# Performance work log

Hardware: AMD Instinct MI355X
Metric: run time of the kernel (lower is better)

## Reference

```python
import jax, jax.numpy as jnp
import numpy as np

N = 8192       # tokens = batch x seq
D = 2048       # d_model
H = 2048       # per-expert hidden size
E = 8          # num_experts
TOP_K = 2


def setup_inputs() -> dict:
    key = jax.random.key(0)
    ks = jax.random.split(key, 6)
    x = jax.random.normal(ks[0], (N, D), dtype=jnp.float32)
    expert_weights = jax.random.uniform(ks[1], (N, TOP_K), dtype=jnp.float32)
    expert_indices = jax.random.randint(ks[2], (N, TOP_K), 0, E, dtype=jnp.int32)
    batch_size_per_expert = jnp.bincount(expert_indices.reshape(-1), length=E).astype(jnp.int32)
    scale = 0.02
    w1 = jax.random.normal(ks[3], (E, D, H), dtype=jnp.float32) * scale
    w2 = jax.random.normal(ks[4], (E, H, D), dtype=jnp.float32) * scale
    w3 = jax.random.normal(ks[5], (E, D, H), dtype=jnp.float32) * scale
    return {"x": x, "expert_weights": expert_weights, "expert_indices": expert_indices,
            "batch_size_per_expert": batch_size_per_expert, "w1": w1, "w2": w2, "w3": w3}


def reference(x, expert_weights, expert_indices, batch_size_per_expert, w1, w2, w3):
    """Math-equivalent to ParallelMLP.forward_once (non-EP path):
    sort tokens by expert, run per-expert SwiGLU MLP, unpermute and combine
    with top-k routing weights. Output does not depend on the sort order,
    so we express it as: out[t] = sum_k w[t,k] * expert_{idx[t,k]}(x[t]).
    """
    n, d = x.shape
    e = w1.shape[0]
    # Dense combine weights (n, E): scatter top-k routing weights.
    cw = jnp.zeros((n, e), x.dtype).at[jnp.arange(n)[:, None], expert_indices].add(expert_weights)
    out = jnp.zeros_like(x)
    for i in range(e):  # small fixed expert count
        h = jax.nn.silu(x @ w1[i]) * (x @ w3[i])  # (n, H) SwiGLU
        out = out + cw[:, i:i + 1] * (h @ w2[i])
    return out
```

## Files before the change

### kernel.cpp

```cpp
#include <hip/hip_runtime.h>
#include <stdint.h>

typedef unsigned short u16;
typedef __attribute__((ext_vector_type(8))) short s16x8;
typedef __attribute__((ext_vector_type(8))) unsigned short u16x8;
typedef __attribute__((ext_vector_type(4))) float f32x4;

#define N_TOK 8192
#define DDIM 2048
#define HDIM 2048
#define NROWS 16384
#define PADROWS 16640
#define MAXTILES 72
#define KTILES 32

#define W1T_OFF    0ull
#define W3T_OFF    67108864ull
#define W2T_OFF    134217728ull
#define XBF_OFF    201326592ull
#define HS_OFF     234881024ull
#define ROWTOK_OFF 303038464ull
#define POS_OFF    303107072ull
#define META_OFF   303172608ull
#define RES_OFF    0ull
#define WS_NEED    303172736ull

__device__ __forceinline__ u16 f2bf(float f) {
  union { float f; unsigned u; } v; v.f = f;
  unsigned r = v.u + 0x7fffu + ((v.u >> 16) & 1u);
  return (u16)(r >> 16);
}
__device__ __forceinline__ float bf2f(u16 u) {
  union { unsigned u; float f; } v; v.u = ((unsigned)u) << 16; return v.f;
}
__device__ __forceinline__ void gload_lds16(const u16* g, u16* l) {
  __builtin_amdgcn_global_load_lds(
      (const __attribute__((address_space(1))) unsigned int*)g,
      (__attribute__((address_space(3))) unsigned int*)l, 16, 0, 0);
}

__global__ void r1_kernel(const int* __restrict__ bsz, int* __restrict__ meta,
                          int* __restrict__ rowtok) {
  if (threadIdx.x == 0) {
    int off = 0, tbv = 0;
    meta[8] = 0; meta[17] = 0;
    for (int e = 0; e < 8; ++e) {
      meta[e] = 0;
      int c = bsz[e];
      off += c;  meta[9 + e] = off;
      tbv += (c + 255) >> 8; meta[18 + e] = tbv;
    }
  }
  for (int p = NROWS + (int)threadIdx.x; p < PADROWS; p += 256) rowtok[p] = 0;
}

__global__ void r2_kernel(const int* __restrict__ eidx, int* __restrict__ meta,
                          int* __restrict__ rowtok, int* __restrict__ posOf) {
  int i = blockIdx.x * 256 + threadIdx.x;
  int e = eidx[i];
  int p = atomicAdd(&meta[e], 1);
  int row = meta[8 + e] + p;
  rowtok[row] = i >> 1;
  posOf[i] = row;
}

__global__ void convert_x_kernel(const float* __restrict__ x, u16* __restrict__ xbf) {
  long long c = blockIdx.x * 256 + threadIdx.x;
  const float4 v0 = *(const float4*)&x[c * 8];
  const float4 v1 = *(const float4*)&x[c * 8 + 4];
  u16x8 u;
  u[0] = f2bf(v0.x); u[1] = f2bf(v0.y); u[2] = f2bf(v0.z); u[3] = f2bf(v0.w);
  u[4] = f2bf(v1.x); u[5] = f2bf(v1.y); u[6] = f2bf(v1.z); u[7] = f2bf(v1.w);
  *(u16x8*)&xbf[c * 8] = u;
}

__global__ __launch_bounds__(256) void transpose_cvt_kernel(
    const float* __restrict__ w1, const float* __restrict__ w2, const float* __restrict__ w3,
    u16* __restrict__ w1T, u16* __restrict__ w2T, u16* __restrict__ w3T) {
  __shared__ float tile[64][65];
  int z = blockIdx.z;
  const float* src; u16* dst;
  if (z < 8)        { src = w1 + (size_t)z * 4194304;        dst = w1T + (size_t)z * 4194304; }
  else if (z < 16)  { src = w3 + (size_t)(z - 8) * 4194304;  dst = w3T + (size_t)(z - 8) * 4194304; }
  else              { src = w2 + (size_t)(z - 16) * 4194304; dst = w2T + (size_t)(z - 16) * 4194304; }
  int r0 = blockIdx.y * 64, c0 = blockIdx.x * 64;
  int tid = threadIdx.x;
  int lr = tid >> 4, lc4 = (tid & 15) * 4;
#pragma unroll
  for (int i = 0; i < 4; ++i) {
    const float4 v = *(const float4*)&src[(size_t)(r0 + lr + i * 16) * 2048 + c0 + lc4];
    tile[lr + i * 16][lc4 + 0] = v.x; tile[lr + i * 16][lc4 + 1] = v.y;
    tile[lr + i * 16][lc4 + 2] = v.z; tile[lr + i * 16][lc4 + 3] = v.w;
  }
  __syncthreads();
  int orb = tid >> 3, oc8 = (tid & 7) * 8;
#pragma unroll
  for (int i = 0; i < 2; ++i) {
    int orow = orb + i * 32;
    u16x8 u;
#pragma unroll
    for (int j = 0; j < 8; ++j) u[j] = f2bf(tile[oc8 + j][orow]);
    *(u16x8*)&dst[(size_t)(c0 + orow) * 2048 + r0 + oc8] = u;
  }
}

template<int EPI>
__device__ __forceinline__ void gemm_body(
    const u16* __restrict__ A, const u16* __restrict__ B1m, const u16* __restrict__ B3m,
    const int* __restrict__ gather, const int* __restrict__ meta, u16* __restrict__ out) {
  const int* offs = meta + 8;
  const int* tb = meta + 17;

  const int NCOLB = EPI ? 16 : 8;
  const int CG = NCOLB / 4;
  const int nper = (MAXTILES * NCOLB) / 8;
  const int lin = (int)blockIdx.x;
  const int w = (lin & 7) * nper + (lin >> 3);
  const int sb = w >> 5, t5 = w & 31;
  const int tileId = (sb / CG) * 8 + (t5 >> 2);
  const int colb = (sb % CG) * 4 + (t5 & 3);

  if (tileId >= tb[8]) return;
  int e = 0;
#pragma unroll
  for (int qq = 1; qq < 8; ++qq) if (tileId >= tb[qq]) e = qq;
  const int row0 = offs[e] + (tileId - tb[e]) * 256;
  const int vr = offs[e + 1] - row0;

  const int bRowA = EPI ? colb * 128 : colb * 256;
  const int bRowB = EPI ? colb * 128 : colb * 256 + 128;

  __shared__ u16 lds[2][4][8192];

  const int tid = threadIdx.x;
  const int wid = tid >> 6, lane = tid & 63;
  const int lm = lane & 15, kg = lane >> 4;
  const int wr = wid >> 2, wc = wid & 3;

  const u16* pA0[2]; const u16* pA1[2]; const u16* pB1[2]; const u16* pB3[2];
#pragma unroll
  for (int l = 0; l < 2; ++l) {
    int S = (wid * 2 + l) * 64 + lane;
    int r = S >> 3;
    int c8 = ((S & 7) ^ (r & 7)) * 8;
    int ga0 = row0 + r, ga1 = row0 + 128 + r;
    int ta0 = gather ? gather[ga0] : ga0;
    int ta1 = gather ? gather[ga1] : ga1;
    pA0[l] = A + (size_t)ta0 * 2048 + c8;
    pA1[l] = A + (size_t)ta1 * 2048 + c8;
    pB1[l] = B1m + ((size_t)e * 2048 + bRowA + r) * 2048 + c8;
    pB3[l] = B3m + ((size_t)e * 2048 + bRowB + r) * 2048 + c8;
  }

  int fA[2];
  fA[0] = lm * 64 + ((kg) ^ (lm & 7)) * 8;
  fA[1] = lm * 64 + ((4 + kg) ^ (lm & 7)) * 8;

  f32x4 acc1[8][2], acc3[8][2];
  f32x4 z4 = {0.f, 0.f, 0.f, 0.f};
#pragma unroll
  for (int m = 0; m < 8; ++m)
#pragma unroll
    for (int n = 0; n < 2; ++n) { acc1[m][n] = z4; acc3[m][n] = z4; }

#define STG(b, u, P) do { \
    gload_lds16(P[0], &lds[b][u][(wid * 2 + 0) * 512]); \
    gload_lds16(P[1], &lds[b][u][(wid * 2 + 1) * 512]); } while (0)
#define STG_ALL(b) do { STG(b, 0, pA0); STG(b, 1, pA1); \
    STG(b, 2, pB1); STG(b, 3, pB3); } while (0)
#define ADV() do { pA0[0]+=64; pA0[1]+=64; pA1[0]+=64; pA1[1]+=64; \
    pB1[0]+=64; pB1[1]+=64; pB3[0]+=64; pB3[1]+=64; } while (0)

  STG_ALL(0);
  ADV();

  s16x8 a[4][2], b1r[2][2], b3r[2][2];

#define READ_B() do { \
_Pragma("unroll") \
    for (int n = 0; n < 2; ++n) \
_Pragma("unroll") \
      for (int kk = 0; kk < 2; ++kk) { \
        b1r[n][kk] = *(const s16x8*)&lds[cur][2][wc * 2048 + n * 1024 + fA[kk]]; \
        b3r[n][kk] = *(const s16x8*)&lds[cur][3][wc * 2048 + n * 1024 + fA[kk]]; \
      } } while (0)
#define READ_A(half) do { \
_Pragma("unroll") \
    for (int mi = 0; mi < 4; ++mi) \
_Pragma("unroll") \
      for (int kk = 0; kk < 2; ++kk) \
        a[mi][kk] = *(const s16x8*)&lds[cur][wr][((half) * 4 + mi) * 1024 + fA[kk]]; \
    } while (0)
#define MFMA32(half) do { \
    __builtin_amdgcn_s_setprio(1); \
_Pragma("unroll") \
    for (int mi = 0; mi < 4; ++mi) \
_Pragma("unroll") \
      for (int n = 0; n < 2; ++n) { \
        acc1[(half)*4+mi][n] = __builtin_amdgcn_mfma_f32_16x16x32_bf16(a[mi][0], b1r[n][0], acc1[(half)*4+mi][n], 0, 0, 0); \
        acc1[(half)*4+mi][n] = __builtin_amdgcn_mfma_f32_16x16x32_bf16(a[mi][1], b1r[n][1], acc1[(half)*4+mi][n], 0, 0, 0); \
        acc3[(half)*4+mi][n] = __builtin_amdgcn_mfma_f32_16x16x32_bf16(a[mi][0], b3r[n][0], acc3[(half)*4+mi][n], 0, 0, 0); \
        acc3[(half)*4+mi][n] = __builtin_amdgcn_mfma_f32_16x16x32_bf16(a[mi][1], b3r[n][1], acc3[(half)*4+mi][n], 0, 0, 0); \
      } \
    __builtin_amdgcn_s_setprio(0); } while (0)

  for (int t = 0; t < KTILES - 1; ++t) {
    const int cur = t & 1;
    STG_ALL(cur ^ 1);
    ADV();
    asm volatile("s_waitcnt vmcnt(8)" ::: "memory");
    __builtin_amdgcn_s_barrier();
    READ_A(0);
    READ_B();
    MFMA32(0);
    __builtin_amdgcn_s_barrier();
    READ_A(1);
    MFMA32(1);
    __builtin_amdgcn_s_barrier();
  }
  {
    const int cur = (KTILES - 1) & 1;
    asm volatile("s_waitcnt vmcnt(0)" ::: "memory");
    __builtin_amdgcn_s_barrier();
    READ_A(0);
    READ_B();
    MFMA32(0);
    __builtin_amdgcn_s_barrier();
    READ_A(1);
    MFMA32(1);
  }

#pragma unroll
  for (int m = 0; m < 8; ++m)
#pragma unroll
    for (int n = 0; n < 2; ++n) {
      const int rloc = wr * 128 + m * 16 + kg * 4;
      if (EPI == 1) {
        const int col = colb * 128 + wc * 32 + n * 16 + lm;
#pragma unroll
        for (int rr = 0; rr < 4; ++rr) {
          int rowl = rloc + rr;
          if (rowl < vr) {
            float z = acc1[m][n][rr];
            float h = z / (1.f + __expf(-z)) * acc3[m][n][rr];
            out[(size_t)(row0 + rowl) * 2048 + col] = f2bf(h);
          }
        }
      } else {
        const int col = colb * 256 + wc * 32 + n * 16 + lm;
#pragma unroll
        for (int rr = 0; rr < 4; ++rr) {
          int rowl = rloc + rr;
          if (rowl < vr) {
            out[(size_t)(row0 + rowl) * 2048 + col] = f2bf(acc1[m][n][rr]);
            out[(size_t)(row0 + rowl) * 2048 + col + 128] = f2bf(acc3[m][n][rr]);
          }
        }
      }
    }
#undef STG
#undef STG_ALL
#undef ADV
#undef READ_B
#undef READ_A
#undef MFMA32
}

__global__ __launch_bounds__(512, 2) void gemm1_kernel(
    const u16* __restrict__ A, const u16* __restrict__ B1m, const u16* __restrict__ B3m,
    const int* __restrict__ gather, const int* __restrict__ meta, u16* __restrict__ out) {
  gemm_body<1>(A, B1m, B3m, gather, meta, out);
}
__global__ __launch_bounds__(512, 2) void gemm2_kernel(
    const u16* __restrict__ A, const u16* __restrict__ B1m, const u16* __restrict__ B3m,
    const int* __restrict__ gather, const int* __restrict__ meta, u16* __restrict__ out) {
  gemm_body<0>(A, B1m, B3m, gather, meta, out);
}

__global__ void combine_kernel(const u16* __restrict__ res, const int* __restrict__ posOf,
                               const float* __restrict__ ew, float* __restrict__ out) {
  int c = blockIdx.x * 256 + threadIdx.x;
  int t = c >> 8, dc = (c & 255) * 8;
  int p0 = posOf[2 * t], p1 = posOf[2 * t + 1];
  float wa = ew[2 * t], wb = ew[2 * t + 1];
  u16x8 u0 = *(const u16x8*)&res[(size_t)p0 * 2048 + dc];
  u16x8 u1 = *(const u16x8*)&res[(size_t)p1 * 2048 + dc];
  float4 o0, o1;
  o0.x = wa * bf2f(u0[0]) + wb * bf2f(u1[0]);
  o0.y = wa * bf2f(u0[1]) + wb * bf2f(u1[1]);
  o0.z = wa * bf2f(u0[2]) + wb * bf2f(u1[2]);
  o0.w = wa * bf2f(u0[3]) + wb * bf2f(u1[3]);
  o1.x = wa * bf2f(u0[4]) + wb * bf2f(u1[4]);
  o1.y = wa * bf2f(u0[5]) + wb * bf2f(u1[5]);
  o1.z = wa * bf2f(u0[6]) + wb * bf2f(u1[6]);
  o1.w = wa * bf2f(u0[7]) + wb * bf2f(u1[7]);
  *(float4*)&out[(size_t)t * 2048 + dc] = o0;
  *(float4*)&out[(size_t)t * 2048 + dc + 4] = o1;
}

extern "C" void kernel_launch(void* const* d_in, const int* in_sizes, int n_in,
                              void* d_out, int out_size, void* d_ws, size_t ws_size,
                              hipStream_t stream) {
  const float* x  = (const float*)d_in[0];
  const float* ew = (const float*)d_in[1];
  const int* eidx = (const int*)d_in[2];
  const int* bsz  = (const int*)d_in[3];
  const float* w1 = (const float*)d_in[4];
  const float* w2 = (const float*)d_in[5];
  const float* w3 = (const float*)d_in[6];
  float* out = (float*)d_out;
  char* ws = (char*)d_ws;

  if (ws_size < WS_NEED) {
    hipMemsetAsync(d_out, 0, (size_t)out_size * 4, stream);
    return;
  }

  u16* w1T = (u16*)(ws + W1T_OFF);
  u16* w3T = (u16*)(ws + W3T_OFF);
  u16* w2T = (u16*)(ws + W2T_OFF);
  u16* xbf = (u16*)(ws + XBF_OFF);
  u16* hs  = (u16*)(ws + HS_OFF);
  u16* res = (u16*)(ws + RES_OFF);
  int* rowtok = (int*)(ws + ROWTOK_OFF);
  int* posOf  = (int*)(ws + POS_OFF);
  int* meta   = (int*)(ws + META_OFF);

  r1_kernel<<<1, 256, 0, stream>>>(bsz, meta, rowtok);
  r2_kernel<<<64, 256, 0, stream>>>(eidx, meta, rowtok, posOf);
  convert_x_kernel<<<8192, 256, 0, stream>>>(x, xbf);
  transpose_cvt_kernel<<<dim3(32, 32, 24), 256, 0, stream>>>(w1, w2, w3, w1T, w2T, w3T);
  gemm1_kernel<<<MAXTILES * 16, 512, 0, stream>>>(xbf, w1T, w3T, rowtok, meta, hs);
  gemm2_kernel<<<MAXTILES * 8, 512, 0, stream>>>(hs, w2T, w2T, nullptr, meta, res);
  combine_kernel<<<8192, 256, 0, stream>>>(res, posOf, ew, out);
}
```

Before: 708.8 us.

## Load A operand directly into registers and restage warp tiling to 4x2

The GEMM body no longer stages the gathered A rows through LDS. Each wave now loads its A fragments straight from global memory into registers, double-buffered across K tiles. LDS holds only the B1/B3 weight tiles, which halves shared memory use, and the warp layout changes from 2x4 to 4x2 with 64x64 per-wave output. This removes the LDS round trip and half of each tile's LDS traffic for A, at the cost of uncoalesced 16-byte global loads of gathered rows and a simpler synchronisation scheme that no longer uses explicit vmcnt waits.

```diff
diff --git a/kernel.cpp b/kernel.cpp
--- a/kernel.cpp
+++ b/kernel.cpp
@@ -130,113 +130,99 @@
   const int bRowA = EPI ? colb * 128 : colb * 256;
   const int bRowB = EPI ? colb * 128 : colb * 256 + 128;
 
-  __shared__ u16 lds[2][4][8192];
+  __shared__ u16 lds[2][2][8192];
 
   const int tid = threadIdx.x;
   const int wid = tid >> 6, lane = tid & 63;
   const int lm = lane & 15, kg = lane >> 4;
-  const int wr = wid >> 2, wc = wid & 3;
-
-  const u16* pA0[2]; const u16* pA1[2]; const u16* pB1[2]; const u16* pB3[2];
+  const int wr = wid >> 1, wc = wid & 1;
+
+  const u16* pB1[2]; const u16* pB3[2];
 #pragma unroll
   for (int l = 0; l < 2; ++l) {
     int S = (wid * 2 + l) * 64 + lane;
     int r = S >> 3;
     int c8 = ((S & 7) ^ (r & 7)) * 8;
-    int ga0 = row0 + r, ga1 = row0 + 128 + r;
-    int ta0 = gather ? gather[ga0] : ga0;
-    int ta1 = gather ? gather[ga1] : ga1;
-    pA0[l] = A + (size_t)ta0 * 2048 + c8;
-    pA1[l] = A + (size_t)ta1 * 2048 + c8;
     pB1[l] = B1m + ((size_t)e * 2048 + bRowA + r) * 2048 + c8;
     pB3[l] = B3m + ((size_t)e * 2048 + bRowB + r) * 2048 + c8;
+  }
+
+  const u16* pa[4];
+#pragma unroll
+  for (int mi = 0; mi < 4; ++mi) {
+    int grow = row0 + wr * 64 + mi * 16 + lm;
+    int ta = gather ? gather[grow] : grow;
+    pa[mi] = A + (size_t)ta * 2048 + kg * 8;
   }
 
   int fA[2];
   fA[0] = lm * 64 + ((kg) ^ (lm & 7)) * 8;
   fA[1] = lm * 64 + ((4 + kg) ^ (lm & 7)) * 8;
 
-  f32x4 acc1[8][2], acc3[8][2];
+  f32x4 acc1[4][4], acc3[4][4];
   f32x4 z4 = {0.f, 0.f, 0.f, 0.f};
 #pragma unroll
-  for (int m = 0; m < 8; ++m)
-#pragma unroll
-    for (int n = 0; n < 2; ++n) { acc1[m][n] = z4; acc3[m][n] = z4; }
-
-#define STG(b, u, P) do { \
-    gload_lds16(P[0], &lds[b][u][(wid * 2 + 0) * 512]); \
-    gload_lds16(P[1], &lds[b][u][(wid * 2 + 1) * 512]); } while (0)
-#define STG_ALL(b) do { STG(b, 0, pA0); STG(b, 1, pA1); \
-    STG(b, 2, pB1); STG(b, 3, pB3); } while (0)
-#define ADV() do { pA0[0]+=64; pA0[1]+=64; pA1[0]+=64; pA1[1]+=64; \
-    pB1[0]+=64; pB1[1]+=64; pB3[0]+=64; pB3[1]+=64; } while (0)
-
-  STG_ALL(0);
-  ADV();
-
-  s16x8 a[4][2], b1r[2][2], b3r[2][2];
-
-#define READ_B() do { \
+  for (int m = 0; m < 4; ++m)
+#pragma unroll
+    for (int n = 0; n < 4; ++n) { acc1[m][n] = z4; acc3[m][n] = z4; }
+
+  s16x8 aA[4][2], aB[4][2], b[2][2];
+
+#define STG(bf, u, P) do { \
+    gload_lds16(P[0], &lds[bf][u][(wid * 2 + 0) * 512]); \
+    gload_lds16(P[1], &lds[bf][u][(wid * 2 + 1) * 512]); \
+    P[0] += 64; P[1] += 64; } while (0)
+#define LOAD_A(ar) do { \
+_Pragma("unroll") \
+    for (int mi = 0; mi < 4; ++mi) { \
+      ar[mi][0] = *(const s16x8*)(pa[mi]); \
+      ar[mi][1] = *(const s16x8*)(pa[mi] + 32); \
+      pa[mi] += 64; } } while (0)
+#define READ_B2(cur, unit, np) do { \
 _Pragma("unroll") \
     for (int n = 0; n < 2; ++n) \
 _Pragma("unroll") \
-      for (int kk = 0; kk < 2; ++kk) { \
-        b1r[n][kk] = *(const s16x8*)&lds[cur][2][wc * 2048 + n * 1024 + fA[kk]]; \
-        b3r[n][kk] = *(const s16x8*)&lds[cur][3][wc * 2048 + n * 1024 + fA[kk]]; \
-      } } while (0)
-#define READ_A(half) do { \
+      for (int kk = 0; kk < 2; ++kk) \
+        b[n][kk] = *(const s16x8*)&lds[cur][unit][wc * 4096 + ((np) * 2 + n) * 1024 + fA[kk]]; \
+    } while (0)
+#define MFMA16G(ACC, np, ar) do { \
+    __builtin_amdgcn_s_setprio(1); \
 _Pragma("unroll") \
     for (int mi = 0; mi < 4; ++mi) \
 _Pragma("unroll") \
-      for (int kk = 0; kk < 2; ++kk) \
-        a[mi][kk] = *(const s16x8*)&lds[cur][wr][((half) * 4 + mi) * 1024 + fA[kk]]; \
-    } while (0)
-#define MFMA32(half) do { \
-    __builtin_amdgcn_s_setprio(1); \
-_Pragma("unroll") \
-    for (int mi = 0; mi < 4; ++mi) \
-_Pragma("unroll") \
       for (int n = 0; n < 2; ++n) { \
-        acc1[(half)*4+mi][n] = __builtin_amdgcn_mfma_f32_16x16x32_bf16(a[mi][0], b1r[n][0], acc1[(half)*4+mi][n], 0, 0, 0); \
-        acc1[(half)*4+mi][n] = __builtin_amdgcn_mfma_f32_16x16x32_bf16(a[mi][1], b1r[n][1], acc1[(half)*4+mi][n], 0, 0, 0); \
-        acc3[(half)*4+mi][n] = __builtin_amdgcn_mfma_f32_16x16x32_bf16(a[mi][0], b3r[n][0], acc3[(half)*4+mi][n], 0, 0, 0); \
-        acc3[(half)*4+mi][n] = __builtin_amdgcn_mfma_f32_16x16x32_bf16(a[mi][1], b3r[n][1], acc3[(half)*4+mi][n], 0, 0, 0); \
+        ACC[mi][(np) * 2 + n] = __builtin_amdgcn_mfma_f32_16x16x32_bf16(ar[mi][0], b[n][0], ACC[mi][(np) * 2 + n], 0, 0, 0); \
+        ACC[mi][(np) * 2 + n] = __builtin_amdgcn_mfma_f32_16x16x32_bf16(ar[mi][1], b[n][1], ACC[mi][(np) * 2 + n], 0, 0, 0); \
       } \
     __builtin_amdgcn_s_setprio(0); } while (0)
 
-  for (int t = 0; t < KTILES - 1; ++t) {
-    const int cur = t & 1;
-    STG_ALL(cur ^ 1);
-    ADV();
-    asm volatile("s_waitcnt vmcnt(8)" ::: "memory");
-    __builtin_amdgcn_s_barrier();
-    READ_A(0);
-    READ_B();
-    MFMA32(0);
-    __builtin_amdgcn_s_barrier();
-    READ_A(1);
-    MFMA32(1);
-    __builtin_amdgcn_s_barrier();
-  }
-  {
-    const int cur = (KTILES - 1) & 1;
-    asm volatile("s_waitcnt vmcnt(0)" ::: "memory");
-    __builtin_amdgcn_s_barrier();
-    READ_A(0);
-    READ_B();
-    MFMA32(0);
-    __builtin_amdgcn_s_barrier();
-    READ_A(1);
-    MFMA32(1);
-  }
-
-#pragma unroll
-  for (int m = 0; m < 8; ++m)
-#pragma unroll
-    for (int n = 0; n < 2; ++n) {
-      const int rloc = wr * 128 + m * 16 + kg * 4;
+#define TILE(cur, aC, aN, STAGE) do { \
+    if (STAGE) { STG(cur ^ 1, 0, pB1); STG(cur ^ 1, 1, pB3); LOAD_A(aN); } \
+    READ_B2(cur, 0, 0); MFMA16G(acc1, 0, aC); \
+    READ_B2(cur, 0, 1); MFMA16G(acc1, 1, aC); \
+    READ_B2(cur, 1, 0); MFMA16G(acc3, 0, aC); \
+    READ_B2(cur, 1, 1); MFMA16G(acc3, 1, aC); \
+    __syncthreads(); } while (0)
+
+  STG(0, 0, pB1);
+  STG(0, 1, pB3);
+  LOAD_A(aA);
+  __syncthreads();
+
+  for (int t = 0; t < KTILES - 2; t += 2) {
+    TILE(0, aA, aB, 1);
+    TILE(1, aB, aA, 1);
+  }
+  TILE(0, aA, aB, 1);
+  TILE(1, aB, aA, 0);
+
+#pragma unroll
+  for (int m = 0; m < 4; ++m)
+#pragma unroll
+    for (int n = 0; n < 4; ++n) {
+      const int rloc = wr * 64 + m * 16 + kg * 4;
       if (EPI == 1) {
-        const int col = colb * 128 + wc * 32 + n * 16 + lm;
+        const int col = colb * 128 + wc * 64 + n * 16 + lm;
 #pragma unroll
         for (int rr = 0; rr < 4; ++rr) {
           int rowl = rloc + rr;
@@ -247,7 +233,7 @@
           }
         }
       } else {
-        const int col = colb * 256 + wc * 32 + n * 16 + lm;
+        const int col = colb * 256 + wc * 64 + n * 16 + lm;
 #pragma unroll
         for (int rr = 0; rr < 4; ++rr) {
           int rowl = rloc + rr;
@@ -259,11 +245,10 @@
       }
     }
 #undef STG
-#undef STG_ALL
-#undef ADV
-#undef READ_B
-#undef READ_A
-#undef MFMA32
+#undef LOAD_A
+#undef READ_B2
+#undef MFMA16G
+#undef TILE
 }
 
 __global__ __launch_bounds__(512, 2) void gemm1_kernel(
```

After: 905.8 us. 1.28x slower.

## Split GEMM K-loop into four phases interleaving LDS reads, global prefetch and MFMA

Applied to the files above, without the earlier changes.

Restructures the double-buffered GEMM main loop into four sub-phases per K-tile, each working on one accumulator (acc1 or acc3) and one M-half. Global-to-LDS prefetches for the next tile are split into two groups issued between phases, with finer vmcnt/lgkmcnt waits and extra barriers. The loop is unrolled by two so buffer indices are compile-time constants. The aim is to overlap LDS reads and global loads with MFMA more evenly, at the cost of more barriers per tile and a more fragile waitcnt sequence.

```diff
diff --git a/kernel.cpp b/kernel.cpp
--- a/kernel.cpp
+++ b/kernel.cpp
@@ -163,72 +163,101 @@
 #pragma unroll
     for (int n = 0; n < 2; ++n) { acc1[m][n] = z4; acc3[m][n] = z4; }
 
+  s16x8 a[4][2], b1r[2][2], b3r[2][2];
+
 #define STG(b, u, P) do { \
     gload_lds16(P[0], &lds[b][u][(wid * 2 + 0) * 512]); \
-    gload_lds16(P[1], &lds[b][u][(wid * 2 + 1) * 512]); } while (0)
-#define STG_ALL(b) do { STG(b, 0, pA0); STG(b, 1, pA1); \
-    STG(b, 2, pB1); STG(b, 3, pB3); } while (0)
-#define ADV() do { pA0[0]+=64; pA0[1]+=64; pA1[0]+=64; pA1[1]+=64; \
-    pB1[0]+=64; pB1[1]+=64; pB3[0]+=64; pB3[1]+=64; } while (0)
-
-  STG_ALL(0);
-  ADV();
-
-  s16x8 a[4][2], b1r[2][2], b3r[2][2];
-
-#define READ_B() do { \
-_Pragma("unroll") \
-    for (int n = 0; n < 2; ++n) \
-_Pragma("unroll") \
-      for (int kk = 0; kk < 2; ++kk) { \
-        b1r[n][kk] = *(const s16x8*)&lds[cur][2][wc * 2048 + n * 1024 + fA[kk]]; \
-        b3r[n][kk] = *(const s16x8*)&lds[cur][3][wc * 2048 + n * 1024 + fA[kk]]; \
-      } } while (0)
-#define READ_A(half) do { \
+    gload_lds16(P[1], &lds[b][u][(wid * 2 + 1) * 512]); \
+    P[0] += 64; P[1] += 64; } while (0)
+#define READ_A(cur, half) do { \
 _Pragma("unroll") \
     for (int mi = 0; mi < 4; ++mi) \
 _Pragma("unroll") \
       for (int kk = 0; kk < 2; ++kk) \
         a[mi][kk] = *(const s16x8*)&lds[cur][wr][((half) * 4 + mi) * 1024 + fA[kk]]; \
     } while (0)
-#define MFMA32(half) do { \
+#define READ_B1(cur) do { \
+_Pragma("unroll") \
+    for (int n = 0; n < 2; ++n) \
+_Pragma("unroll") \
+      for (int kk = 0; kk < 2; ++kk) \
+        b1r[n][kk] = *(const s16x8*)&lds[cur][2][wc * 2048 + n * 1024 + fA[kk]]; \
+    } while (0)
+#define READ_B3(cur) do { \
+_Pragma("unroll") \
+    for (int n = 0; n < 2; ++n) \
+_Pragma("unroll") \
+      for (int kk = 0; kk < 2; ++kk) \
+        b3r[n][kk] = *(const s16x8*)&lds[cur][3][wc * 2048 + n * 1024 + fA[kk]]; \
+    } while (0)
+#define MFMA16(ACC, half, B) do { \
     __builtin_amdgcn_s_setprio(1); \
 _Pragma("unroll") \
     for (int mi = 0; mi < 4; ++mi) \
 _Pragma("unroll") \
       for (int n = 0; n < 2; ++n) { \
-        acc1[(half)*4+mi][n] = __builtin_amdgcn_mfma_f32_16x16x32_bf16(a[mi][0], b1r[n][0], acc1[(half)*4+mi][n], 0, 0, 0); \
-        acc1[(half)*4+mi][n] = __builtin_amdgcn_mfma_f32_16x16x32_bf16(a[mi][1], b1r[n][1], acc1[(half)*4+mi][n], 0, 0, 0); \
-        acc3[(half)*4+mi][n] = __builtin_amdgcn_mfma_f32_16x16x32_bf16(a[mi][0], b3r[n][0], acc3[(half)*4+mi][n], 0, 0, 0); \
-        acc3[(half)*4+mi][n] = __builtin_amdgcn_mfma_f32_16x16x32_bf16(a[mi][1], b3r[n][1], acc3[(half)*4+mi][n], 0, 0, 0); \
+        ACC[(half)*4+mi][n] = __builtin_amdgcn_mfma_f32_16x16x32_bf16(a[mi][0], B[n][0], ACC[(half)*4+mi][n], 0, 0, 0); \
+        ACC[(half)*4+mi][n] = __builtin_amdgcn_mfma_f32_16x16x32_bf16(a[mi][1], B[n][1], ACC[(half)*4+mi][n], 0, 0, 0); \
       } \
     __builtin_amdgcn_s_setprio(0); } while (0)
-
-  for (int t = 0; t < KTILES - 1; ++t) {
-    const int cur = t & 1;
-    STG_ALL(cur ^ 1);
-    ADV();
-    asm volatile("s_waitcnt vmcnt(8)" ::: "memory");
-    __builtin_amdgcn_s_barrier();
-    READ_A(0);
-    READ_B();
-    MFMA32(0);
-    __builtin_amdgcn_s_barrier();
-    READ_A(1);
-    MFMA32(1);
-    __builtin_amdgcn_s_barrier();
-  }
-  {
-    const int cur = (KTILES - 1) & 1;
-    asm volatile("s_waitcnt vmcnt(0)" ::: "memory");
-    __builtin_amdgcn_s_barrier();
-    READ_A(0);
-    READ_B();
-    MFMA32(0);
-    __builtin_amdgcn_s_barrier();
-    READ_A(1);
-    MFMA32(1);
-  }
+#define ABAR() asm volatile("s_barrier" ::: "memory")
+#define LGKM0_FENCE() do { asm volatile("s_waitcnt lgkmcnt(0)" ::: "memory"); \
+    __builtin_amdgcn_sched_barrier(0); } while (0)
+
+#define TILE_MAIN(cur) do { \
+     \
+    READ_A(cur, 0); READ_B1(cur); \
+    STG(cur ^ 1, 0, pA0); STG(cur ^ 1, 2, pB1); \
+    asm volatile("s_waitcnt vmcnt(4) lgkmcnt(8)" ::: "memory"); \
+    ABAR(); LGKM0_FENCE(); \
+    MFMA16(acc1, 0, b1r); \
+    ABAR(); \
+     \
+    READ_B3(cur); \
+    STG(cur ^ 1, 1, pA1); STG(cur ^ 1, 3, pB3); \
+    ABAR(); LGKM0_FENCE(); \
+    MFMA16(acc3, 0, b3r); \
+    ABAR(); \
+     \
+    READ_A(cur, 1); \
+    ABAR(); LGKM0_FENCE(); \
+    MFMA16(acc1, 1, b1r); \
+    ABAR(); \
+     \
+    asm volatile("s_waitcnt vmcnt(2)" ::: "memory"); \
+    ABAR(); \
+    MFMA16(acc3, 1, b3r); \
+    ABAR(); } while (0)
+
+#define TILE_LAST(cur) do { \
+    READ_A(cur, 0); READ_B1(cur); \
+    asm volatile("s_waitcnt vmcnt(0) lgkmcnt(8)" ::: "memory"); \
+    ABAR(); LGKM0_FENCE(); \
+    MFMA16(acc1, 0, b1r); \
+    ABAR(); \
+    READ_B3(cur); \
+    ABAR(); LGKM0_FENCE(); \
+    MFMA16(acc3, 0, b3r); \
+    ABAR(); \
+    READ_A(cur, 1); \
+    ABAR(); LGKM0_FENCE(); \
+    MFMA16(acc1, 1, b1r); \
+    ABAR(); \
+    MFMA16(acc3, 1, b3r); } while (0)
+
+  STG(0, 0, pA0);
+  STG(0, 2, pB1);
+  STG(0, 1, pA1);
+  STG(0, 3, pB3);
+  asm volatile("s_waitcnt vmcnt(2)" ::: "memory");
+  ABAR();
+
+  for (int t = 0; t < KTILES - 2; t += 2) {
+    TILE_MAIN(0);
+    TILE_MAIN(1);
+  }
+  TILE_MAIN(0);
+  TILE_LAST(1);
 
 #pragma unroll
   for (int m = 0; m < 8; ++m)
@@ -259,11 +288,14 @@
       }
     }
 #undef STG
-#undef STG_ALL
-#undef ADV
-#undef READ_B
 #undef READ_A
-#undef MFMA32
+#undef READ_B1
+#undef READ_B3
+#undef MFMA16
+#undef ABAR
+#undef LGKM0_FENCE
+#undef TILE_MAIN
+#undef TILE_LAST
 }
 
 __global__ __launch_bounds__(512, 2) void gemm1_kernel(
```

Measured after the change: 691.6 us (median of 2 runs). -2.4%, faster.
